# Performance work log

Hardware: AMD Instinct MI355X
Metric: run time of the kernel (lower is better)

Reference implementation:

```python
import jax, jax.numpy as jnp
import numpy as np
from jax import lax


def _bilinear_gather(img, ys, xs):
    """img: [B,H,W,C]; ys,xs: [B,K,H,W] fractional coords. Zero padding outside.
    Returns [B,K,H,W,C]."""
    B, H, W, C = img.shape
    y0 = jnp.floor(ys)
    x0 = jnp.floor(xs)
    wy = (ys - y0)[..., None]
    wx = (xs - x0)[..., None]
    y0i = y0.astype(jnp.int32)
    x0i = x0.astype(jnp.int32)
    flat = img.reshape(B, H * W, C)

    def gather(yi, xi):
        valid = (yi >= 0) & (yi < H) & (xi >= 0) & (xi < W)
        yc = jnp.clip(yi, 0, H - 1)
        xc = jnp.clip(xi, 0, W - 1)
        idx = (yc * W + xc).reshape(B, -1, 1)
        g = jnp.take_along_axis(flat, idx, axis=1).reshape(yi.shape + (C,))
        return g * valid[..., None].astype(img.dtype)

    v00 = gather(y0i, x0i)
    v01 = gather(y0i, x0i + 1)
    v10 = gather(y0i + 1, x0i)
    v11 = gather(y0i + 1, x0i + 1)
    one = jnp.asarray(1.0, img.dtype)
    return (v00 * (one - wy) * (one - wx) + v01 * (one - wy) * wx
            + v10 * wy * (one - wx) + v11 * wy * wx)


def _forward(x, w_off, b_off, w_def, b_def, w_attn, b_attn):
    B, Cin, H, W = x.shape
    Cout = w_def.shape[0]
    # offset conv: 3x3, pad 1 -> [B, 18, H, W]
    off = lax.conv_general_dilated(x, w_off, (1, 1), ((1, 1), (1, 1)))
    off = off + b_off[None, :, None, None]
    off = off.reshape(B, 9, 2, H, W)
    dy = off[:, :, 0]  # [B,9,H,W], torchvision order: (dy, dx) per kernel pt
    dx = off[:, :, 1]
    # kernel point grid, row-major over (kh, kw)
    ky, kx = jnp.meshgrid(jnp.arange(3), jnp.arange(3), indexing='ij')
    ky = ky.reshape(9).astype(x.dtype)
    kx = kx.reshape(9).astype(x.dtype)
    ii = jnp.arange(H, dtype=x.dtype)
    jj = jnp.arange(W, dtype=x.dtype)
    # sample position = (out_pos - pad + k) + offset, pad=1, stride=1
    ys = ii[None, None, :, None] - 1.0 + ky[None, :, None, None] + dy
    xs = jj[None, None, None, :] - 1.0 + kx[None, :, None, None] + dx
    img = x.transpose(0, 2, 3, 1)  # [B,H,W,Cin]
    sampled = _bilinear_gather(img, ys, xs)  # [B,9,H,W,Cin]
    wk = w_def.reshape(Cout, Cin, 9)  # row-major kernel pts match ky/kx
    out = jnp.einsum('bkhwc,ock->bohw', sampled, wk) + b_def[None, :, None, None]
    # spatial attention: 1x1 conv -> sigmoid gate
    attn = jnp.einsum('bchw,oc->bohw', out, w_attn[:, :, 0, 0]) + b_attn[None, :, None, None]
    out = out * jax.nn.sigmoid(attn)
    return jax.nn.relu(out)


def setup_inputs() -> dict:
    key = jax.random.key(0)
    ks = jax.random.split(key, 5)
    B, C, H, W = 4, 128, 128, 128
    x = jax.random.normal(ks[0], (B, C, H, W), dtype=jnp.float32)
    w_off = jax.random.normal(ks[1], (18, C, 3, 3), dtype=jnp.float32) * 0.02
    b_off = jnp.zeros((18,), dtype=jnp.float32)
    w_def = jax.random.normal(ks[2], (C, C, 3, 3), dtype=jnp.float32) * (1.0 / np.sqrt(C * 9))
    b_def = jnp.zeros((C,), dtype=jnp.float32)
    w_attn = jax.random.normal(ks[3], (1, C, 1, 1), dtype=jnp.float32) * (1.0 / np.sqrt(C))
    b_attn = jnp.zeros((1,), dtype=jnp.float32)
    return {"x": x, "w_off": w_off, "b_off": b_off, "w_def": w_def,
            "b_def": b_def, "w_attn": w_attn, "b_attn": b_attn}


def reference(x, w_off, b_off, w_def, b_def, w_attn, b_attn):
    return _forward(x, w_off, b_off, w_def, b_def, w_attn, b_attn)
```

## Files before the change

### kernel.cpp

```cpp
#include <hip/hip_runtime.h>
#include <math.h>

#define Cch 128
#define Hh 128
#define Ww 128
#define HW (Hh * Ww)

typedef __attribute__((ext_vector_type(8))) short short8;
typedef __attribute__((ext_vector_type(4))) float float4v;
typedef __attribute__((ext_vector_type(2))) float float2v;
typedef __attribute__((ext_vector_type(4))) unsigned int uint4v;

__device__ __forceinline__ unsigned short f2bf(float f) {
    unsigned u = __float_as_uint(f);
    return (unsigned short)((u + 0x8000u) >> 16);
}
__device__ __forceinline__ float2v up2(unsigned u) {
    return (float2v){__uint_as_float(u << 16), __uint_as_float(u & 0xffff0000u)};
}
__device__ __forceinline__ unsigned packbf2(float lo, float hi) {
    unsigned a = __float_as_uint(lo), b = __float_as_uint(hi);
    return ((a + 0x8000u) >> 16) | ((b + 0x8000u) & 0xffff0000u);
}

__global__ __launch_bounds__(256) void transpose_x_bf16(const float* __restrict__ x,
                                                        unsigned short* __restrict__ xt) {
    __shared__ float tile[32][33];
    int b  = blockIdx.z;
    int c0 = blockIdx.y * 32;
    int p0 = blockIdx.x * 32;
    int tx = threadIdx.x, ty = threadIdx.y;
    const float* xb = x + (size_t)b * Cch * HW;
    unsigned short* xtb = xt + (size_t)b * HW * Cch;
    #pragma unroll
    for (int i = 0; i < 32; i += 8)
        tile[ty + i][tx] = __builtin_nontemporal_load(&xb[(size_t)(c0 + ty + i) * HW + p0 + tx]);
    __syncthreads();
    #pragma unroll
    for (int i = 0; i < 32; i += 8)
        xtb[(size_t)(p0 + ty + i) * Cch + c0 + tx] = f2bf(tile[tx][ty + i]);
}

#define NFB (9 * 4 * 8 * 64 * 8)
#define NFO (9 * 4 * 2 * 64 * 8)
__global__ __launch_bounds__(256) void build_frags(const float* __restrict__ w_def,
                                                   const float* __restrict__ w_off,
                                                   unsigned short* __restrict__ wfB,
                                                   unsigned short* __restrict__ wfO) {
    int idx = blockIdx.x * 256 + threadIdx.x;
    if (idx < NFB) {
        int j = idx & 7, lane = (idx >> 3) & 63, t = (idx >> 9) & 7;
        int q = (idx >> 12) & 3, k = idx >> 14;
        int c = 32 * q + 8 * (lane >> 4) + j;
        int o = 16 * t + (lane & 15);
        wfB[idx] = f2bf(w_def[(size_t)(o * Cch + c) * 9 + k]);
    } else if (idx < NFB + NFO) {
        int i2 = idx - NFB;
        int j = i2 & 7, lane = (i2 >> 3) & 63, t = (i2 >> 9) & 1;
        int q = (i2 >> 10) & 3, k = i2 >> 12;
        int c = 32 * q + 8 * (lane >> 4) + j;
        int o = 16 * t + (lane & 15);
        wfO[i2] = (o < 18) ? f2bf(w_off[(size_t)(o * Cch + c) * 9 + k]) : (unsigned short)0;
    }
}

__device__ __forceinline__ void blk_map(int blk, int& b, int& h, int& w0) {
    int xcd = blk & 7;
    b = xcd >> 1;
    int seg = ((xcd & 1) << 8) | (blk >> 3);
    h  = seg >> 2;
    w0 = (seg & 3) << 5;
}

__global__ __launch_bounds__(128, 2) void fused_srt(const unsigned short* __restrict__ xt,
                                                    const unsigned short* __restrict__ wfB,
                                                    const unsigned short* __restrict__ wfO,
                                                    const float* __restrict__ b_off,
                                                    const float* __restrict__ b_def,
                                                    const float* __restrict__ w_attn,
                                                    const float* __restrict__ b_attn,
                                                    float* __restrict__ out) {
    __shared__ float4v red[2 * 8 * 64];
    __shared__ float   offs[32 * 18];
    __shared__ uint4v  smw[2 * 4 * 64];
    int b, h, w0;
    blk_map(blockIdx.x, b, h, w0);
    int tid  = threadIdx.x;
    int wave = tid >> 6;
    int lane = tid & 63;
    int col  = lane & 15;
    int s    = lane >> 4;
    int spx  = lane >> 2;
    int sch  = lane & 3;
    int cbase = 64 * wave;
    int csrt  = cbase + sch * 8;
    int wbase = wave * 256;
    int rIdx  = wbase + ((lane & 15) * 4 + (lane >> 4));

    const unsigned short* xtb = xt + (size_t)b * HW * Cch;

    {
        float4v acc2[2][2];
        #pragma unroll
        for (int pt = 0; pt < 2; ++pt)
            #pragma unroll
            for (int t = 0; t < 2; ++t) {
                int o = 16 * t + col;
                float bv = (wave == 0 && o < 18) ? b_off[o] : 0.0f;
                acc2[pt][t] = (float4v){bv, bv, bv, bv};
            }

        #pragma unroll
        for (int k = 0; k < 9; ++k) {
            int y = h + (k / 3) - 1;
            bool vy = (y >= 0) && (y < Hh);
            int yc = min(max(y, 0), Hh - 1);
            int dxk = (k % 3) - 1;
            int  ofs[2];
            bool val[2];
            #pragma unroll
            for (int pt = 0; pt < 2; ++pt) {
                int px = w0 + 16 * pt + spx;
                int xs = px + dxk;
                val[pt] = vy && (xs >= 0) && (xs < Ww);
                int xc  = min(max(xs, 0), Ww - 1);
                ofs[pt] = (yc * Ww + xc) * Cch + csrt;
            }
            #pragma unroll
            for (int pt = 0; pt < 2; ++pt)
                #pragma unroll
                for (int qq = 0; qq < 2; ++qq) {
                    uint4v av = *(const uint4v*)(xtb + ofs[pt] + 32 * qq);
                    if (!val[pt]) av = (uint4v){0u, 0u, 0u, 0u};
                    smw[wbase + (pt * 2 + qq) * 64 + lane] = av;
                }
            short8 aa[2][2];
            #pragma unroll
            for (int pt = 0; pt < 2; ++pt)
                #pragma unroll
                for (int qq = 0; qq < 2; ++qq)
                    aa[pt][qq] = __builtin_bit_cast(short8, smw[rIdx + (pt * 2 + qq) * 64]);
            #pragma unroll
            for (int qq = 0; qq < 2; ++qq) {
                int q = 2 * wave + qq;
                #pragma unroll
                for (int t = 0; t < 2; ++t) {
                    short8 bv = *(const short8*)(wfO + ((size_t)((k * 4 + q) * 2 + t) * 64 + lane) * 8);
                    #pragma unroll
                    for (int pt = 0; pt < 2; ++pt)
                        acc2[pt][t] = __builtin_amdgcn_mfma_f32_16x16x32_bf16(aa[pt][qq], bv, acc2[pt][t], 0, 0, 0);
                }
            }
        }
        if (wave == 1) {
            #pragma unroll
            for (int pt = 0; pt < 2; ++pt)
                #pragma unroll
                for (int t = 0; t < 2; ++t)
                    red[(pt * 2 + t) * 64 + lane] = acc2[pt][t];
        }
        __syncthreads();
        if (wave == 0) {
            #pragma unroll
            for (int pt = 0; pt < 2; ++pt)
                #pragma unroll
                for (int t = 0; t < 2; ++t) {
                    float4v v = acc2[pt][t] + red[(pt * 2 + t) * 64 + lane];
                    int o = 16 * t + col;
                    if (o < 18) {
                        #pragma unroll
                        for (int r = 0; r < 4; ++r)
                            offs[(16 * pt + 4 * s + r) * 18 + o] = v[r];
                    }
                }
        }
        __syncthreads();
    }

    float4v acc[2][8];
    #pragma unroll
    for (int pt = 0; pt < 2; ++pt)
        #pragma unroll
        for (int t = 0; t < 8; ++t) {
            float bv = (wave == 0) ? b_def[16 * t + col] : 0.0f;
            acc[pt][t] = (float4v){bv, bv, bv, bv};
        }

    int    oaddr[2][4];
    float  wxy[2][4];
    uint4v u[2][8];

#define CALC_TAP(K_) do {                                                    \
    int ky = ((K_) * 11) >> 5;                                               \
    int kx = (K_) - 3 * ky;                                                  \
    _Pragma("unroll")                                                        \
    for (int pt = 0; pt < 2; ++pt) {                                         \
        int pxl = 16 * pt + spx;                                             \
        int px  = w0 + pxl;                                                  \
        float2 dv = *(const float2*)&offs[pxl * 18 + 2 * (K_)];              \
        float ys = (float)(h - 1 + ky) + dv.x;                               \
        float xs = (float)(px - 1 + kx) + dv.y;                              \
        float y0f = floorf(ys), x0f = floorf(xs);                            \
        float wy = ys - y0f, wx = xs - x0f;                                  \
        int y0 = (int)y0f, x0 = (int)x0f;                                    \
        bool vy0 = (y0 >= 0) && (y0 < Hh);                                   \
        bool vy1 = (y0 + 1 >= 0) && (y0 + 1 < Hh);                           \
        bool vx0 = (x0 >= 0) && (x0 < Ww);                                   \
        bool vx1 = (x0 + 1 >= 0) && (x0 + 1 < Ww);                           \
        int y0c = min(max(y0, 0), Hh - 1), y1c = min(max(y0 + 1, 0), Hh - 1);\
        int x0c = min(max(x0, 0), Ww - 1), x1c = min(max(x0 + 1, 0), Ww - 1);\
        wxy[pt][0] = vx0 ? (1.0f - wx) : 0.0f;                               \
        wxy[pt][1] = vx1 ? wx : 0.0f;                                        \
        wxy[pt][2] = vy0 ? (1.0f - wy) : 0.0f;                               \
        wxy[pt][3] = vy1 ? wy : 0.0f;                                        \
        oaddr[pt][0] = (y0c * Ww + x0c) * Cch + csrt;                        \
        oaddr[pt][1] = (y0c * Ww + x1c) * Cch + csrt;                        \
        oaddr[pt][2] = (y1c * Ww + x0c) * Cch + csrt;                        \
        oaddr[pt][3] = (y1c * Ww + x1c) * Cch + csrt;                        \
    }                                                                        \
} while (0)

#define LOAD_TAP() do {                                                      \
    _Pragma("unroll")                                                        \
    for (int pt = 0; pt < 2; ++pt)                                           \
        _Pragma("unroll")                                                    \
        for (int qq = 0; qq < 2; ++qq)                                       \
            _Pragma("unroll")                                                \
            for (int c4 = 0; c4 < 4; ++c4)                                   \
                u[pt][qq * 4 + c4] =                                         \
                    *(const uint4v*)(xtb + oaddr[pt][c4] + 32 * qq);         \
} while (0)

    CALC_TAP(0);
    LOAD_TAP();

    #pragma unroll
    for (int k = 0; k < 9; ++k) {
        const unsigned short* wk = wfB + (size_t)k * 16384 + (size_t)(2 * wave) * 4096;
        short8 bva[8], bvb[8];
        #pragma unroll
        for (int t = 0; t < 8; ++t) {
            bva[t] = *(const short8*)(wk + (size_t)t * 512 + (size_t)lane * 8);
            bvb[t] = *(const short8*)(wk + 4096 + (size_t)t * 512 + (size_t)lane * 8);
        }
        #pragma unroll
        for (int pt = 0; pt < 2; ++pt) {
            float2v A0 = (float2v){wxy[pt][0], wxy[pt][0]};
            float2v A1 = (float2v){wxy[pt][1], wxy[pt][1]};
            float2v B0 = (float2v){wxy[pt][2], wxy[pt][2]};
            float2v B1 = (float2v){wxy[pt][3], wxy[pt][3]};
            #pragma unroll
            for (int qq = 0; qq < 2; ++qq) {
                uint4v res;
                #pragma unroll
                for (int j = 0; j < 4; ++j) {
                    float2v p00 = up2(u[pt][qq * 4 + 0][j]);
                    float2v p01 = up2(u[pt][qq * 4 + 1][j]);
                    float2v p10 = up2(u[pt][qq * 4 + 2][j]);
                    float2v p11 = up2(u[pt][qq * 4 + 3][j]);
                    float2v t0 = __builtin_elementwise_fma(A1, p01, A0 * p00);
                    float2v t1 = __builtin_elementwise_fma(A1, p11, A0 * p10);
                    float2v rr = __builtin_elementwise_fma(B1, t1, B0 * t0);
                    res[j] = packbf2(rr.x, rr.y);
                }
                smw[wbase + (pt * 2 + qq) * 64 + lane] = res;
            }
        }
        if (k < 8) {
            CALC_TAP(k + 1);
            LOAD_TAP();
        }
        short8 afr[2][2];
        #pragma unroll
        for (int pt = 0; pt < 2; ++pt)
            #pragma unroll
            for (int qq = 0; qq < 2; ++qq)
                afr[pt][qq] = __builtin_bit_cast(short8, smw[rIdx + (pt * 2 + qq) * 64]);
        #pragma unroll
        for (int t = 0; t < 8; ++t) {
            acc[0][t] = __builtin_amdgcn_mfma_f32_16x16x32_bf16(afr[0][0], bva[t], acc[0][t], 0, 0, 0);
            acc[1][t] = __builtin_amdgcn_mfma_f32_16x16x32_bf16(afr[1][0], bva[t], acc[1][t], 0, 0, 0);
        }
        #pragma unroll
        for (int t = 0; t < 8; ++t) {
            acc[0][t] = __builtin_amdgcn_mfma_f32_16x16x32_bf16(afr[0][1], bvb[t], acc[0][t], 0, 0, 0);
            acc[1][t] = __builtin_amdgcn_mfma_f32_16x16x32_bf16(afr[1][1], bvb[t], acc[1][t], 0, 0, 0);
        }
    }
#undef CALC_TAP
#undef LOAD_TAP

    if (wave == 1) {
        #pragma unroll
        for (int pt = 0; pt < 2; ++pt)
            #pragma unroll
            for (int t = 0; t < 8; ++t)
                red[(pt * 8 + t) * 64 + lane] = acc[pt][t];
    }
    __syncthreads();
    if (wave == 0) {
        #pragma unroll
        for (int pt = 0; pt < 2; ++pt)
            #pragma unroll
            for (int t = 0; t < 8; ++t)
                acc[pt][t] += red[(pt * 8 + t) * 64 + lane];

        float wA[8];
        #pragma unroll
        for (int t = 0; t < 8; ++t) wA[t] = w_attn[16 * t + col];
        float battn = b_attn[0];
        #pragma unroll
        for (int pt = 0; pt < 2; ++pt) {
            float sig[4];
            #pragma unroll
            for (int r = 0; r < 4; ++r) {
                float pr = 0.0f;
                #pragma unroll
                for (int t = 0; t < 8; ++t) pr = fmaf(acc[pt][t][r], wA[t], pr);
                #pragma unroll
                for (int m = 1; m < 16; m <<= 1) pr += __shfl_xor(pr, m, 64);
                sig[r] = 1.0f / (1.0f + expf(-(pr + battn)));
            }
            #pragma unroll
            for (int t = 0; t < 8; ++t) {
                int o = 16 * t + col;
                float4v v;
                #pragma unroll
                for (int r = 0; r < 4; ++r)
                    v[r] = fmaxf(acc[pt][t][r] * sig[r], 0.0f);
                float* dst = out + ((size_t)(b * Cch + o)) * HW + h * Ww + w0 + 16 * pt + 4 * s;
                __builtin_nontemporal_store(v, (float4v*)dst);
            }
        }
    }
}

extern "C" void kernel_launch(void* const* d_in, const int* in_sizes, int n_in,
                              void* d_out, int out_size, void* d_ws, size_t ws_size,
                              hipStream_t stream) {
    const float* x      = (const float*)d_in[0];
    const float* w_off  = (const float*)d_in[1];
    const float* b_off  = (const float*)d_in[2];
    const float* w_def  = (const float*)d_in[3];
    const float* b_def  = (const float*)d_in[4];
    const float* w_attn = (const float*)d_in[5];
    const float* b_attn = (const float*)d_in[6];
    float* out = (float*)d_out;

    char* ws = (char*)d_ws;
    unsigned short* xt  = (unsigned short*)ws;
    unsigned short* wfB = (unsigned short*)(ws + 16777216);
    unsigned short* wfO = (unsigned short*)(ws + 17072128);

    transpose_x_bf16<<<dim3(512, 4, 4), dim3(32, 8), 0, stream>>>(x, xt);
    build_frags<<<720, 256, 0, stream>>>(w_def, w_off, wfB, wfO);
    fused_srt<<<2048, 128, 0, stream>>>(xt, wfB, wfO, b_off, b_def, w_attn, b_attn, out);
}
```

Before: 157.9 us.

## Alias LDS buffers for higher occupancy and replace tiled transpose with direct bf16 packing

The shared-memory arrays in the fused kernel are merged into one aliased raw buffer. The final reduction scratch now overlaps the weight staging area, with an extra barrier to keep them separate, and launch bounds are raised to allow three blocks per CU. The shared-memory tiled transpose is replaced by a kernel where each thread loads 8 channels for one pixel and writes one 16-byte packed bf16 vector, which avoids LDS and the barrier. Output stores become regular rather than nontemporal. The tighter register budget from the higher launch bound risks spills, and the added barrier costs some latency.

```diff
diff --git a/kernel.cpp b/kernel.cpp
--- a/kernel.cpp
+++ b/kernel.cpp
@@ -23,22 +23,22 @@
     return ((a + 0x8000u) >> 16) | ((b + 0x8000u) & 0xffff0000u);
 }
 
-__global__ __launch_bounds__(256) void transpose_x_bf16(const float* __restrict__ x,
-                                                        unsigned short* __restrict__ xt) {
-    __shared__ float tile[32][33];
-    int b  = blockIdx.z;
-    int c0 = blockIdx.y * 32;
-    int p0 = blockIdx.x * 32;
-    int tx = threadIdx.x, ty = threadIdx.y;
-    const float* xb = x + (size_t)b * Cch * HW;
-    unsigned short* xtb = xt + (size_t)b * HW * Cch;
+__global__ __launch_bounds__(256) void pack_x_bf16(const float* __restrict__ x,
+                                                   unsigned short* __restrict__ xt) {
+    int t   = threadIdx.x;
+    int blk = blockIdx.x;
+    int b   = blk >> 10;
+    int p   = ((blk & 1023) << 4) + (t >> 4);
+    int c0  = (t & 15) * 8;
+    const float* xb = x + (size_t)b * Cch * HW + p;
+    float v[8];
     #pragma unroll
-    for (int i = 0; i < 32; i += 8)
-        tile[ty + i][tx] = __builtin_nontemporal_load(&xb[(size_t)(c0 + ty + i) * HW + p0 + tx]);
-    __syncthreads();
+    for (int i = 0; i < 8; ++i)
+        v[i] = __builtin_nontemporal_load(&xb[(size_t)(c0 + i) * HW]);
+    uint4v r;
     #pragma unroll
-    for (int i = 0; i < 32; i += 8)
-        xtb[(size_t)(p0 + ty + i) * Cch + c0 + tx] = f2bf(tile[tx][ty + i]);
+    for (int j = 0; j < 4; ++j) r[j] = packbf2(v[2 * j], v[2 * j + 1]);
+    *(uint4v*)(xt + (size_t)b * HW * Cch + (size_t)p * Cch + c0) = r;
 }
 
 #define NFB (9 * 4 * 8 * 64 * 8)
@@ -72,7 +72,7 @@
     w0 = (seg & 3) << 5;
 }
 
-__global__ __launch_bounds__(128, 2) void fused_srt(const unsigned short* __restrict__ xt,
+__global__ __launch_bounds__(128, 3) void fused_srt(const unsigned short* __restrict__ xt,
                                                     const unsigned short* __restrict__ wfB,
                                                     const unsigned short* __restrict__ wfO,
                                                     const float* __restrict__ b_off,
@@ -80,9 +80,12 @@
                                                     const float* __restrict__ w_attn,
                                                     const float* __restrict__ b_attn,
                                                     float* __restrict__ out) {
-    __shared__ float4v red[2 * 8 * 64];
-    __shared__ float   offs[32 * 18];
-    __shared__ uint4v  smw[2 * 4 * 64];
+    __shared__ __align__(16) char lds_raw[18688];
+    float4v* red3 = (float4v*)lds_raw;
+    float4v* red1 = (float4v*)(lds_raw + 8192);
+    uint4v*  smw  = (uint4v*)lds_raw;
+    float*   offs = (float*)(lds_raw + 16384);
+
     int b, h, w0;
     blk_map(blockIdx.x, b, h, w0);
     int tid  = threadIdx.x;
@@ -157,7 +160,7 @@
             for (int pt = 0; pt < 2; ++pt)
                 #pragma unroll
                 for (int t = 0; t < 2; ++t)
-                    red[(pt * 2 + t) * 64 + lane] = acc2[pt][t];
+                    red1[(pt * 2 + t) * 64 + lane] = acc2[pt][t];
         }
         __syncthreads();
         if (wave == 0) {
@@ -165,7 +168,7 @@
             for (int pt = 0; pt < 2; ++pt)
                 #pragma unroll
                 for (int t = 0; t < 2; ++t) {
-                    float4v v = acc2[pt][t] + red[(pt * 2 + t) * 64 + lane];
+                    float4v v = acc2[pt][t] + red1[(pt * 2 + t) * 64 + lane];
                     int o = 16 * t + col;
                     if (o < 18) {
                         #pragma unroll
@@ -290,12 +293,13 @@
 #undef CALC_TAP
 #undef LOAD_TAP
 
+    __syncthreads();
     if (wave == 1) {
         #pragma unroll
         for (int pt = 0; pt < 2; ++pt)
             #pragma unroll
             for (int t = 0; t < 8; ++t)
-                red[(pt * 8 + t) * 64 + lane] = acc[pt][t];
+                red3[(pt * 8 + t) * 64 + lane] = acc[pt][t];
     }
     __syncthreads();
     if (wave == 0) {
@@ -303,7 +307,7 @@
         for (int pt = 0; pt < 2; ++pt)
             #pragma unroll
             for (int t = 0; t < 8; ++t)
-                acc[pt][t] += red[(pt * 8 + t) * 64 + lane];
+                acc[pt][t] += red3[(pt * 8 + t) * 64 + lane];
 
         float wA[8];
         #pragma unroll
@@ -329,7 +333,7 @@
                 for (int r = 0; r < 4; ++r)
                     v[r] = fmaxf(acc[pt][t][r] * sig[r], 0.0f);
                 float* dst = out + ((size_t)(b * Cch + o)) * HW + h * Ww + w0 + 16 * pt + 4 * s;
-                __builtin_nontemporal_store(v, (float4v*)dst);
+                *(float4v*)dst = v;
             }
         }
     }
@@ -352,7 +356,7 @@
     unsigned short* wfB = (unsigned short*)(ws + 16777216);
     unsigned short* wfO = (unsigned short*)(ws + 17072128);
 
-    transpose_x_bf16<<<dim3(512, 4, 4), dim3(32, 8), 0, stream>>>(x, xt);
+    pack_x_bf16<<<4096, 256, 0, stream>>>(x, xt);
     build_frags<<<720, 256, 0, stream>>>(w_def, w_off, wfB, wfO);
     fused_srt<<<2048, 128, 0, stream>>>(xt, wfB, wfO, b_off, b_def, w_attn, b_attn, out);
 }
```

New measurement: 199.5 us. 26.3% more time.
